# Kernel optimization log

Hardware: AMD Instinct MI355X
Metric: run time of the kernel (lower is better)

The kernel has to match this reference:

```python
import jax, jax.numpy as jnp
import numpy as np


def gru_layer(x, W_ih, W_hh, b_ih, b_hh):
    """PyTorch-semantics GRU over a full sequence.
    x: [B, T, F]; W_ih: [3H, F]; W_hh: [3H, H]; biases: [3H].
    Gate order (r, z, n) per torch.nn.GRU. Returns [B, T, H].
    """
    B, T, _ = x.shape
    H = W_hh.shape[1]
    # Precompute input projections for all timesteps as one big GEMM: [B, T, 3H]
    xg = jnp.einsum('btf,gf->btg', x, W_ih) + b_ih

    def step(h, xg_t):
        gh = h @ W_hh.T + b_hh                      # [B, 3H]
        xr, xz, xn = jnp.split(xg_t, 3, axis=-1)
        hr, hz, hn = jnp.split(gh, 3, axis=-1)
        r = jax.nn.sigmoid(xr + hr)
        z = jax.nn.sigmoid(xz + hz)
        n = jnp.tanh(xn + r * hn)
        h_new = (1.0 - z) * n + z * h
        return h_new, h_new

    h0 = jnp.zeros((B, H), dtype=x.dtype)
    _, hs = jax.lax.scan(step, h0, jnp.swapaxes(xg, 0, 1))  # hs: [T, B, H]
    return jnp.swapaxes(hs, 0, 1)


def setup_inputs() -> dict:
    key = jax.random.key(0)
    ks = jax.random.split(key, 16)
    B, T, F = 512, 256, 64
    H1, H2, H3 = 256, 128, 64

    def w(k, shape, fan_in):
        s = 1.0 / np.sqrt(fan_in)
        return jax.random.uniform(k, shape, jnp.float32, -s, s)

    return {
        'x': jax.random.normal(ks[0], (B, T, F), jnp.float32),
        'W_ih1': w(ks[1], (3 * H1, F), H1),
        'W_hh1': w(ks[2], (3 * H1, H1), H1),
        'b_ih1': w(ks[3], (3 * H1,), H1),
        'b_hh1': w(ks[4], (3 * H1,), H1),
        'W_ih2': w(ks[5], (3 * H2, H1), H2),
        'W_hh2': w(ks[6], (3 * H2, H2), H2),
        'b_ih2': w(ks[7], (3 * H2,), H2),
        'b_hh2': w(ks[8], (3 * H2,), H2),
        'W_ih3': w(ks[9], (3 * H3, H2), H3),
        'W_hh3': w(ks[10], (3 * H3, H3), H3),
        'b_ih3': w(ks[11], (3 * H3,), H3),
        'b_hh3': w(ks[12], (3 * H3,), H3),
        'W_dense': w(ks[13], (1, H3), H3),
        'b_dense': w(ks[14], (1,), H3),
    }


def reference(x, W_ih1, W_hh1, b_ih1, b_hh1,
              W_ih2, W_hh2, b_ih2, b_hh2,
              W_ih3, W_hh3, b_ih3, b_hh3,
              W_dense, b_dense):
    # Dropout layers act as identity in eval mode.
    h = gru_layer(x, W_ih1, W_hh1, b_ih1, b_hh1)   # [B, T, 256]
    h = gru_layer(h, W_ih2, W_hh2, b_ih2, b_hh2)   # [B, T, 128]
    h = gru_layer(h, W_ih3, W_hh3, b_ih3, b_hh3)   # [B, T, 64]
    last = h[:, -1, :]                              # [B, 64]
    return last @ W_dense.T + b_dense               # [B, 1]
```

## Files before the change

kernel.cpp:

```cpp
#include <hip/hip_runtime.h>
#include <cstddef>

typedef _Float16 f16x8 __attribute__((ext_vector_type(8)));
typedef _Float16 f16x4 __attribute__((ext_vector_type(4)));
typedef short    s16x8 __attribute__((ext_vector_type(8)));
typedef short    s16x4 __attribute__((ext_vector_type(4)));
typedef float    f32x4 __attribute__((ext_vector_type(4)));

#define MFMA_F16(a, b, c) __builtin_amdgcn_mfma_f32_16x16x32_f16((a), (b), (c), 0, 0, 0)

#if __has_builtin(__builtin_amdgcn_rcpf)
__device__ __forceinline__ float fast_rcp(float x) { return __builtin_amdgcn_rcpf(x); }
#else
__device__ __forceinline__ float fast_rcp(float x) { return 1.f / x; }
#endif

__device__ __forceinline__ f16x8 ld8(const short* p) {
  return __builtin_bit_cast(f16x8, *(const s16x8*)p);
}
__device__ __forceinline__ f16x4 ld4(const short* p) {
  return __builtin_bit_cast(f16x4, *(const s16x4*)p);
}

__device__ __forceinline__ void barrier_nodrain() {
  asm volatile("s_waitcnt lgkmcnt(0)" ::: "memory");
  __builtin_amdgcn_s_barrier();
  asm volatile("" ::: "memory");
}

struct CastDesc { const float* src; short* dst; int n; };
struct CastArgs { CastDesc d[7]; };

__global__ void cast_many(CastArgs a) {
  const int tid = blockIdx.x * blockDim.x + threadIdx.x;
  const int stride = gridDim.x * blockDim.x;
#pragma unroll
  for (int j = 0; j < 7; j++) {
    const float* __restrict__ s = a.d[j].src;
    short* __restrict__ o = a.d[j].dst;
    const int n = a.d[j].n;
    for (int i = tid; i < n; i += stride)
      o[i] = __builtin_bit_cast(short, (_Float16)s[i]);
  }
}

template <int K, int NO, int NW, int JT>
__global__ __launch_bounds__(NW * 64, 2)
void xg_gemm(const short* __restrict__ A,
             const short* __restrict__ W,
             const float* __restrict__ bias,
             short* __restrict__ xg,
             int t0, int TC) {
  static_assert(NW * 16 * JT == NO, "wave tiling must cover NO");
  constexpr int T = 256;
  constexpr int TT = 16;
  constexpr int KC = K / 32;
  const int lane = threadIdx.x & 63;
  const int wid  = threadIdx.x >> 6;
  const int p = lane & 15, q = lane >> 4;
  const int bt = blockIdx.x;
  const int tbeg = t0 + blockIdx.y * TT;
  const int j0 = wid * 16 * JT;

  f16x8 wb[JT][KC];
  float bc[JT];
#pragma unroll
  for (int jt = 0; jt < JT; jt++) {
    const int col = j0 + jt * 16 + p;
    bc[jt] = bias[col];
#pragma unroll
    for (int kc = 0; kc < KC; kc++)
      wb[jt][kc] = ld8(W + (size_t)col * K + kc * 32 + q * 8);
  }

  const short* arow = A + ((size_t)(bt * 16 + p) * T + tbeg) * K + q * 8;
  short* outb = xg + ((size_t)bt * TC + (tbeg - t0)) * NO * 16;

  f16x8 a0[KC], a1[KC];
#pragma unroll
  for (int kc = 0; kc < KC; kc++) a0[kc] = ld8(arow + kc * 32);

  auto step = [&](int ti, f16x8 (&ac)[KC], f16x8 (&anx)[KC], bool pf) {
    if (pf) {
#pragma unroll
      for (int kc = 0; kc < KC; kc++)
        anx[kc] = ld8(arow + (size_t)(ti + 1) * K + kc * 32);
    }
    f32x4 acc[JT];
#pragma unroll
    for (int jt = 0; jt < JT; jt++)
      acc[jt] = f32x4{bc[jt], bc[jt], bc[jt], bc[jt]};
#pragma unroll
    for (int kc = 0; kc < KC; kc++)
#pragma unroll
      for (int jt = 0; jt < JT; jt++)
        acc[jt] = MFMA_F16(ac[kc], wb[jt][kc], acc[jt]);
    short* ob = outb + (size_t)ti * NO * 16;
#pragma unroll
    for (int jt = 0; jt < JT; jt++) {
      const int col = j0 + jt * 16 + p;
      s16x4 v;
#pragma unroll
      for (int r = 0; r < 4; r++)
        v[r] = __builtin_bit_cast(short, (_Float16)acc[jt][r]);
      *(s16x4*)&ob[col * 16 + q * 4] = v;
    }
  };

#pragma unroll 1
  for (int ti = 0; ti < TT; ti += 2) {
    step(ti, a0, a1, true);
    step(ti + 1, a1, a0, ti + 2 < TT);
  }
}

template <int H, int NW, int JT, bool NLDS, bool SEQ, int XD>
__global__ __launch_bounds__(NW * 64, (NW / 4 >= 2) ? 2 : 1)
void gru_rec(const short* __restrict__ xg,
             const short* __restrict__ Whh,
             const float* __restrict__ bhh,
             short* __restrict__ hseq,
             float* __restrict__ hstate,
             int t0, int t1, int TC) {
  static_assert(NW * 16 * JT == H, "wave tiling must cover H");
  static_assert(XD == 2 || XD == 4, "XD even for static parity");
  constexpr int T = 256;
  constexpr int KS = H / 32;
  constexpr int HP = H + 8;
  constexpr int NO = 3 * H;

  extern __shared__ __align__(16) short smem[];
  short* wn = smem;
  short* hb = smem + (NLDS ? H * HP : 0);

  const int tid  = threadIdx.x;
  const int lane = tid & 63;
  const int wid  = tid >> 6;
  const int p = lane & 15, q = lane >> 4;
  const int b0 = blockIdx.x * 16;
  const int j0 = wid * 16 * JT;

  if constexpr (NLDS) {
    constexpr int KV = H / 8;
    for (int i = tid; i < H * KV; i += NW * 64) {
      const int row = i / KV, kc = i - row * KV;
      *(s16x8*)&wn[row * HP + kc * 8] =
          *(const s16x8*)&Whh[(size_t)(2 * H + row) * H + kc * 8];
    }
  }
  if (t0 == 0) {
    for (int i = tid; i < 16 * HP; i += NW * 64) hb[i] = 0;
  } else {
    for (int i = tid; i < 16 * H; i += NW * 64) {
      const int row = i / H, col = i - row * H;
      hb[row * HP + col] =
          __builtin_bit_cast(short, (_Float16)hstate[(size_t)(b0 + row) * H + col]);
    }
  }

  f16x8 wr[JT][NLDS ? 2 : 3][KS];
#pragma unroll
  for (int jt = 0; jt < JT; jt++) {
    const int col = j0 + jt * 16 + p;
#pragma unroll
    for (int g = 0; g < (NLDS ? 2 : 3); g++)
#pragma unroll
      for (int k = 0; k < KS; k++)
        wr[jt][g][k] = ld8(Whh + (size_t)(g * H + col) * H + k * 32 + q * 8);
  }
  float bhr[JT], bhz[JT], bhn[JT];
  int wrow[JT];
#pragma unroll
  for (int jt = 0; jt < JT; jt++) {
    const int col = j0 + jt * 16 + p;
    wrow[jt] = col;
    bhr[jt] = bhh[col];
    bhz[jt] = bhh[H + col];
    bhn[jt] = bhh[2 * H + col];
  }

  float hprev[JT][4];
#pragma unroll
  for (int jt = 0; jt < JT; jt++)
#pragma unroll
    for (int r = 0; r < 4; r++)
      hprev[jt][r] = (t0 == 0) ? 0.f
                   : hstate[(size_t)(b0 + q * 4 + r) * H + (j0 + jt * 16 + p)];

  const size_t sbase = (size_t)blockIdx.x * TC * NO * 16;
  int loff[JT][3];
#pragma unroll
  for (int jt = 0; jt < JT; jt++)
#pragma unroll
    for (int g = 0; g < 3; g++)
      loff[jt][g] = (g * H + j0 + jt * 16 + p) * 16 + q * 4;

  f16x4 xb[XD][JT][3];
#pragma unroll
  for (int u = 0; u < XD; u++)
#pragma unroll
    for (int jt = 0; jt < JT; jt++)
#pragma unroll
      for (int g = 0; g < 3; g++)
        xb[u][jt][g] = ld4(xg + sbase + (size_t)u * NO * 16 + loff[jt][g]);

  __syncthreads();

  const int steps = t1 - t0;
#pragma unroll 1
  for (int sb = 0; sb < steps; sb += XD) {
#pragma unroll
    for (int u = 0; u < XD; u++) {
      const int s = sb + u;
      const int t = t0 + s;
      short* hbc = hb + (u & 1) * 16 * HP;
      short* hbn = hb + ((u & 1) ^ 1) * 16 * HP;

      f32x4 ar[JT], az[JT], an[JT];
#pragma unroll
      for (int jt = 0; jt < JT; jt++) {
#pragma unroll
        for (int r = 0; r < 4; r++) {
          ar[jt][r] = (float)xb[u][jt][0][r];
          az[jt][r] = (float)xb[u][jt][1][r];
        }
        an[jt] = f32x4{0.f, 0.f, 0.f, 0.f};
      }
#pragma unroll
      for (int k = 0; k < KS; k++) {
        const f16x8 ahk = ld8(&hbc[p * HP + k * 32 + q * 8]);
#pragma unroll
        for (int jt = 0; jt < JT; jt++) {
          ar[jt] = MFMA_F16(ahk, wr[jt][0][k], ar[jt]);
          az[jt] = MFMA_F16(ahk, wr[jt][1][k], az[jt]);
          if constexpr (NLDS) {
            const f16x8 wnk = ld8(&wn[wrow[jt] * HP + k * 32 + q * 8]);
            an[jt] = MFMA_F16(ahk, wnk, an[jt]);
          } else {
            an[jt] = MFMA_F16(ahk, wr[jt][2][k], an[jt]);
          }
        }
      }
#pragma unroll
      for (int jt = 0; jt < JT; jt++) {
        const int col = j0 + jt * 16 + p;
#pragma unroll
        for (int r = 0; r < 4; r++) {
          const int bm = q * 4 + r;
          const float rpre = ar[jt][r] + bhr[jt];
          const float zpre = az[jt][r] + bhz[jt];
          const float rg = fast_rcp(1.f + __expf(-rpre));
          const float zg = fast_rcp(1.f + __expf(-zpre));
          const float xnv = (float)xb[u][jt][2][r];
          const float narg = xnv + rg * (an[jt][r] + bhn[jt]);
          const float e2 = __expf(2.f * narg);
          const float ng = 1.f - 2.f * fast_rcp(e2 + 1.f);
          const float hnew = (1.f - zg) * ng + zg * hprev[jt][r];
          hprev[jt][r] = hnew;
          const _Float16 hf = (_Float16)hnew;
          hbn[bm * HP + col] = __builtin_bit_cast(short, hf);
          if constexpr (SEQ)
            hseq[((size_t)(b0 + bm) * T + t) * H + col] = __builtin_bit_cast(short, hf);
        }
      }
      if (t == t1 - 1) {
#pragma unroll
        for (int jt = 0; jt < JT; jt++)
#pragma unroll
          for (int r = 0; r < 4; r++)
            hstate[(size_t)(b0 + q * 4 + r) * H + (j0 + jt * 16 + p)] = hprev[jt][r];
      }
      {
        const size_t s2 = sbase + (size_t)(s + XD) * NO * 16;
#pragma unroll
        for (int jt = 0; jt < JT; jt++)
#pragma unroll
          for (int g = 0; g < 3; g++)
            xb[u][jt][g] = ld4(xg + s2 + loff[jt][g]);
      }
      barrier_nodrain();
    }
  }
}

__global__ __launch_bounds__(512, 1)
void rec23(const short* __restrict__ xg2,
           const short* __restrict__ Whh2,
           const float* __restrict__ bhh2,
           const short* __restrict__ Wih3,
           const short* __restrict__ Whh3,
           const float* __restrict__ bih3,
           const float* __restrict__ bhh3,
           float* __restrict__ hs2,
           float* __restrict__ hs3,
           int t0, int t1, int TC) {
  constexpr int H2 = 128, H3 = 64;
  constexpr int HP2 = H2 + 8, HP3 = H3 + 8;
  constexpr int NO = 3 * H2;
  __shared__ __align__(16) short hb2[2][16][HP2];
  __shared__ __align__(16) short hb3[2][16][HP3];

  const int tid = threadIdx.x;
  const int lane = tid & 63, wid = tid >> 6;
  const int p = lane & 15, q = lane >> 4;
  const int bt = blockIdx.x, b0 = bt * 16;
  const int col2 = wid * 16 + p;
  const int col3 = (wid & 3) * 16 + p;
  const bool act3 = wid < 4;

  if (t0 == 0) {
    for (int i = tid; i < 2 * 16 * HP2; i += 512) (&hb2[0][0][0])[i] = 0;
    for (int i = tid; i < 2 * 16 * HP3; i += 512) (&hb3[0][0][0])[i] = 0;
  } else {
    for (int i = tid; i < 16 * H2; i += 512) {
      const int r = i / H2, c = i - r * H2;
      hb2[0][r][c] = __builtin_bit_cast(short, (_Float16)hs2[(size_t)(b0 + r) * H2 + c]);
    }
    for (int i = tid; i < 16 * H3; i += 512) {
      const int r = i / H3, c = i - r * H3;
      hb3[0][r][c] = __builtin_bit_cast(short, (_Float16)hs3[(size_t)(b0 + r) * H3 + c]);
    }
  }

  f16x8 w2[3][4];
#pragma unroll
  for (int g = 0; g < 3; g++)
#pragma unroll
    for (int k = 0; k < 4; k++)
      w2[g][k] = ld8(Whh2 + (size_t)(g * H2 + col2) * H2 + k * 32 + q * 8);
  const float br2 = bhh2[col2], bz2 = bhh2[H2 + col2], bn2 = bhh2[2 * H2 + col2];

  f16x8 wi3[3][4], wh3[3][2];
  float br3 = 0.f, bz3 = 0.f, bn3x = 0.f, bn3h = 0.f;
  if (act3) {
#pragma unroll
    for (int g = 0; g < 3; g++) {
#pragma unroll
      for (int k = 0; k < 4; k++)
        wi3[g][k] = ld8(Wih3 + (size_t)(g * H3 + col3) * H2 + k * 32 + q * 8);
#pragma unroll
      for (int k = 0; k < 2; k++)
        wh3[g][k] = ld8(Whh3 + (size_t)(g * H3 + col3) * H3 + k * 32 + q * 8);
    }
    br3 = bih3[col3] + bhh3[col3];
    bz3 = bih3[H3 + col3] + bhh3[H3 + col3];
    bn3x = bih3[2 * H3 + col3];
    bn3h = bhh3[2 * H3 + col3];
  }

  float h2p[4], h3p[4];
#pragma unroll
  for (int r = 0; r < 4; r++) {
    h2p[r] = (t0 == 0) ? 0.f : hs2[(size_t)(b0 + q * 4 + r) * H2 + col2];
    h3p[r] = (!act3 || t0 == 0) ? 0.f : hs3[(size_t)(b0 + q * 4 + r) * H3 + col3];
  }

  const size_t sbase = (size_t)bt * TC * NO * 16;
  int loff[3];
#pragma unroll
  for (int g = 0; g < 3; g++) loff[g] = (g * H2 + col2) * 16 + q * 4;
  f16x4 xb[2][3];
#pragma unroll
  for (int u = 0; u < 2; u++)
#pragma unroll
    for (int g = 0; g < 3; g++)
      xb[u][g] = ld4(xg2 + sbase + (size_t)u * NO * 16 + loff[g]);

  __syncthreads();

  const int steps = t1 - t0;
#pragma unroll 1
  for (int sb = 0; sb < steps; sb += 2) {
#pragma unroll
    for (int u = 0; u < 2; ++u) {
      const int s = sb + u;
      const int t = t0 + s;
      f32x4 ar, az, an;
#pragma unroll
      for (int r = 0; r < 4; r++) { ar[r] = (float)xb[u][0][r]; az[r] = (float)xb[u][1][r]; }
      an = f32x4{0.f, 0.f, 0.f, 0.f};
#pragma unroll
      for (int k = 0; k < 4; k++) {
        const f16x8 ahk = ld8(&hb2[u][p][k * 32 + q * 8]);
        ar = MFMA_F16(ahk, w2[0][k], ar);
        az = MFMA_F16(ahk, w2[1][k], az);
        an = MFMA_F16(ahk, w2[2][k], an);
      }
#pragma unroll
      for (int r = 0; r < 4; r++) {
        const int bm = q * 4 + r;
        const float rg = fast_rcp(1.f + __expf(-(ar[r] + br2)));
        const float zg = fast_rcp(1.f + __expf(-(az[r] + bz2)));
        const float narg = (float)xb[u][2][r] + rg * (an[r] + bn2);
        const float e2 = __expf(2.f * narg);
        const float ng = 1.f - 2.f * fast_rcp(e2 + 1.f);
        const float hnew = (1.f - zg) * ng + zg * h2p[r];
        h2p[r] = hnew;
        hb2[u ^ 1][bm][col2] = __builtin_bit_cast(short, (_Float16)hnew);
        if (t == t1 - 1) hs2[(size_t)(b0 + bm) * H2 + col2] = hnew;
      }
      {
        const size_t s2 = sbase + (size_t)(s + 2) * NO * 16;
#pragma unroll
        for (int g = 0; g < 3; g++) xb[u][g] = ld4(xg2 + s2 + loff[g]);
      }
      barrier_nodrain();
      if (act3) {
        f32x4 a3r{0.f,0.f,0.f,0.f}, a3z{0.f,0.f,0.f,0.f},
              a3x{0.f,0.f,0.f,0.f}, a3h{0.f,0.f,0.f,0.f};
#pragma unroll
        for (int k = 0; k < 4; k++) {
          const f16x8 a2k = ld8(&hb2[u ^ 1][p][k * 32 + q * 8]);
          a3r = MFMA_F16(a2k, wi3[0][k], a3r);
          a3z = MFMA_F16(a2k, wi3[1][k], a3z);
          a3x = MFMA_F16(a2k, wi3[2][k], a3x);
        }
#pragma unroll
        for (int k = 0; k < 2; k++) {
          const f16x8 a3k = ld8(&hb3[u][p][k * 32 + q * 8]);
          a3r = MFMA_F16(a3k, wh3[0][k], a3r);
          a3z = MFMA_F16(a3k, wh3[1][k], a3z);
          a3h = MFMA_F16(a3k, wh3[2][k], a3h);
        }
#pragma unroll
        for (int r = 0; r < 4; r++) {
          const int bm = q * 4 + r;
          const float rg = fast_rcp(1.f + __expf(-(a3r[r] + br3)));
          const float zg = fast_rcp(1.f + __expf(-(a3z[r] + bz3)));
          const float narg = a3x[r] + bn3x + rg * (a3h[r] + bn3h);
          const float e2 = __expf(2.f * narg);
          const float ng = 1.f - 2.f * fast_rcp(e2 + 1.f);
          const float hnew = (1.f - zg) * ng + zg * h3p[r];
          h3p[r] = hnew;
          hb3[u ^ 1][bm][col3] = __builtin_bit_cast(short, (_Float16)hnew);
          if (t == t1 - 1) hs3[(size_t)(b0 + bm) * H3 + col3] = hnew;
        }
      }
    }
  }
}

__global__ void dense_kernel(const float* __restrict__ hl, const float* __restrict__ Wd,
                             const float* __restrict__ bd, float* __restrict__ out) {
  const int b = blockIdx.x * 64 + threadIdx.x;
  float a = bd[0];
#pragma unroll
  for (int k = 0; k < 64; k++) a = fmaf(hl[b * 64 + k], Wd[k], a);
  out[b] = a;
}

extern "C" void kernel_launch(void* const* d_in, const int* in_sizes, int n_in,
                              void* d_out, int out_size, void* d_ws, size_t ws_size,
                              hipStream_t stream) {
  constexpr int B = 512, T = 256, F = 64;
  constexpr int H1 = 256, H2 = 128, H3 = 64;
  constexpr int M = B * T;

  const float* x     = (const float*)d_in[0];
  const float* W_ih1 = (const float*)d_in[1];
  const float* W_hh1 = (const float*)d_in[2];
  const float* b_ih1 = (const float*)d_in[3];
  const float* b_hh1 = (const float*)d_in[4];
  const float* W_ih2 = (const float*)d_in[5];
  const float* W_hh2 = (const float*)d_in[6];
  const float* b_ih2 = (const float*)d_in[7];
  const float* b_hh2 = (const float*)d_in[8];
  const float* W_ih3 = (const float*)d_in[9];
  const float* W_hh3 = (const float*)d_in[10];
  const float* b_ih3 = (const float*)d_in[11];
  const float* b_hh3 = (const float*)d_in[12];
  const float* W_d   = (const float*)d_in[13];
  const float* b_d   = (const float*)d_in[14];
  float* out = (float*)d_out;

  char* ws = (char*)d_ws;
  size_t off = 0;
  auto alloc = [&](size_t bytes) -> char* {
    char* pp = ws + off;
    off = (off + bytes + 255) & ~(size_t)255;
    return pp;
  };

  const int nx    = M * F;
  const int nwih1 = 3 * H1 * F,  nwhh1 = 3 * H1 * H1;
  const int nwih2 = 3 * H2 * H1, nwhh2 = 3 * H2 * H2;
  const int nwih3 = 3 * H3 * H2, nwhh3 = 3 * H3 * H3;

  short* xh   = (short*)alloc((size_t)nx * 2);
  short* wih1 = (short*)alloc((size_t)nwih1 * 2);
  short* whh1 = (short*)alloc((size_t)nwhh1 * 2);
  short* wih2 = (short*)alloc((size_t)nwih2 * 2);
  short* whh2 = (short*)alloc((size_t)nwhh2 * 2);
  short* wih3 = (short*)alloc((size_t)nwih3 * 2);
  short* whh3 = (short*)alloc((size_t)nwhh3 * 2);
  short* h1   = (short*)alloc((size_t)M * H1 * 2);
  float* hs1  = (float*)alloc((size_t)B * H1 * 4);
  float* hs2  = (float*)alloc((size_t)B * H2 * 4);
  float* hs3  = (float*)alloc((size_t)B * H3 * 4);
  short* xgbuf = (short*)(ws + off);
  const size_t avail = (ws_size > off) ? (ws_size - off) : 0;
  (void)n_in; (void)in_sizes; (void)out_size;

  CastArgs ca;
  ca.d[0] = {x, xh, nx};
  ca.d[1] = {W_ih1, wih1, nwih1};
  ca.d[2] = {W_hh1, whh1, nwhh1};
  ca.d[3] = {W_ih2, wih2, nwih2};
  ca.d[4] = {W_hh2, whh2, nwhh2};
  ca.d[5] = {W_ih3, wih3, nwih3};
  ca.d[6] = {W_hh3, whh3, nwhh3};
  cast_many<<<1024, 256, 0, stream>>>(ca);

  auto pick_tc = [&](int NO, int XD) -> int {
    for (int tc = T; tc >= 32; tc >>= 1) {
      size_t need = (size_t)(B / 16) * tc * NO * 16 * 2
                  + (size_t)XD * NO * 16 * 2 + 256;
      if (need <= avail) return tc;
    }
    return 16;
  };

  constexpr int SM1 = (H1 + 2 * 16) * (H1 + 8) * 2;
  auto* r1 = gru_rec<H1, 8, 2, true, true, 2>;
  (void)hipFuncSetAttribute((const void*)r1, hipFuncAttributeMaxDynamicSharedMemorySize, SM1);

  {
    const int TC = pick_tc(3 * H1, 2);
    for (int t0 = 0; t0 < T; t0 += TC) {
      xg_gemm<F, 3 * H1, 4, 12><<<dim3(B / 16, TC / 16), 4 * 64, 0, stream>>>(
          xh, wih1, b_ih1, xgbuf, t0, TC);
      r1<<<B / 16, 8 * 64, SM1, stream>>>(xgbuf, whh1, b_hh1, h1, hs1, t0, t0 + TC, TC);
    }
  }
  {
    const int TC = pick_tc(3 * H2, 2);
    for (int t0 = 0; t0 < T; t0 += TC) {
      xg_gemm<H1, 3 * H2, 8, 3><<<dim3(B / 16, TC / 16), 8 * 64, 0, stream>>>(
          h1, wih2, b_ih2, xgbuf, t0, TC);
      rec23<<<B / 16, 512, 0, stream>>>(xgbuf, whh2, b_hh2, wih3, whh3, b_ih3, b_hh3,
                                        hs2, hs3, t0, t0 + TC, TC);
    }
  }

  dense_kernel<<<B / 64, 64, 0, stream>>>(hs3, W_d, b_d, out);
}
```

Baseline: 946.9 us.

## Overlap next-chunk input GEMM with recurrence via fused kernels and double-buffered ring

Fuses the input-projection GEMM for chunk c+1 into the same launch as the recurrence for chunk c. Extra blocks compute the next xg slot into a two-slot ring buffer while 32 blocks run the serial GRU recurrence, so the GEMM work fills otherwise idle CUs. It also folds b_ih and b_hh for the r/z gates into a combined bias computed in the cast kernel, removing per-step bias adds. In layer 1 it keeps the first four K-chunks of the n-gate weights in registers and the rest in LDS, which shrinks shared memory per block. The cost is higher register and LDS pressure in the fused kernel and a fixed chunk size of 64 steps.

```diff
diff --git a/kernel.cpp b/kernel.cpp
--- a/kernel.cpp
+++ b/kernel.cpp
@@ -9,6 +9,9 @@
 
 #define MFMA_F16(a, b, c) __builtin_amdgcn_mfma_f32_16x16x32_f16((a), (b), (c), 0, 0, 0)
 
+constexpr int GB = 512, GT = 256, GF = 64;
+constexpr int H1 = 256, H2 = 128, H3 = 64;
+
 #if __has_builtin(__builtin_amdgcn_rcpf)
 __device__ __forceinline__ float fast_rcp(float x) { return __builtin_amdgcn_rcpf(x); }
 #else
@@ -29,7 +32,11 @@
 }
 
 struct CastDesc { const float* src; short* dst; int n; };
-struct CastArgs { CastDesc d[7]; };
+struct CastArgs {
+  CastDesc d[7];
+  const float* bih1; const float* bhh1; float* bc1;
+  const float* bih2; const float* bhh2; float* bc2;
+};
 
 __global__ void cast_many(CastArgs a) {
   const int tid = blockIdx.x * blockDim.x + threadIdx.x;
@@ -42,24 +49,22 @@
     for (int i = tid; i < n; i += stride)
       o[i] = __builtin_bit_cast(short, (_Float16)s[i]);
   }
-}
-
-template <int K, int NO, int NW, int JT>
-__global__ __launch_bounds__(NW * 64, 2)
-void xg_gemm(const short* __restrict__ A,
-             const short* __restrict__ W,
-             const float* __restrict__ bias,
-             short* __restrict__ xg,
-             int t0, int TC) {
-  static_assert(NW * 16 * JT == NO, "wave tiling must cover NO");
-  constexpr int T = 256;
+  for (int i = tid; i < 3 * H1; i += stride)
+    a.bc1[i] = a.bih1[i] + (i < 2 * H1 ? a.bhh1[i] : 0.f);
+  for (int i = tid; i < 3 * H2; i += stride)
+    a.bc2[i] = a.bih2[i] + (i < 2 * H2 ? a.bhh2[i] : 0.f);
+}
+
+template <int K, int NO, int JT>
+__device__ __forceinline__ void g_body(const short* __restrict__ A,
+                                       const short* __restrict__ W,
+                                       const float* __restrict__ biasC,
+                                       short* __restrict__ slot, int TC,
+                                       int bt, int trel, int tabs, int tid) {
+  constexpr int KC = K / 32;
   constexpr int TT = 16;
-  constexpr int KC = K / 32;
-  const int lane = threadIdx.x & 63;
-  const int wid  = threadIdx.x >> 6;
+  const int lane = tid & 63, wid = tid >> 6;
   const int p = lane & 15, q = lane >> 4;
-  const int bt = blockIdx.x;
-  const int tbeg = t0 + blockIdx.y * TT;
   const int j0 = wid * 16 * JT;
 
   f16x8 wb[JT][KC];
@@ -67,14 +72,13 @@
 #pragma unroll
   for (int jt = 0; jt < JT; jt++) {
     const int col = j0 + jt * 16 + p;
-    bc[jt] = bias[col];
+    bc[jt] = biasC[col];
 #pragma unroll
     for (int kc = 0; kc < KC; kc++)
       wb[jt][kc] = ld8(W + (size_t)col * K + kc * 32 + q * 8);
   }
-
-  const short* arow = A + ((size_t)(bt * 16 + p) * T + tbeg) * K + q * 8;
-  short* outb = xg + ((size_t)bt * TC + (tbeg - t0)) * NO * 16;
+  const short* arow = A + ((size_t)(bt * 16 + p) * GT + tabs) * K + q * 8;
+  short* outb = slot + ((size_t)bt * TC + trel) * NO * 16;
 
   f16x8 a0[KC], a1[KC];
 #pragma unroll
@@ -114,68 +118,67 @@
   }
 }
 
-template <int H, int NW, int JT, bool NLDS, bool SEQ, int XD>
-__global__ __launch_bounds__(NW * 64, (NW / 4 >= 2) ? 2 : 1)
-void gru_rec(const short* __restrict__ xg,
-             const short* __restrict__ Whh,
-             const float* __restrict__ bhh,
-             short* __restrict__ hseq,
-             float* __restrict__ hstate,
-             int t0, int t1, int TC) {
-  static_assert(NW * 16 * JT == H, "wave tiling must cover H");
-  static_assert(XD == 2 || XD == 4, "XD even for static parity");
-  constexpr int T = 256;
-  constexpr int KS = H / 32;
-  constexpr int HP = H + 8;
-  constexpr int NO = 3 * H;
-
-  extern __shared__ __align__(16) short smem[];
+template <int K, int NO, int JT>
+__global__ __launch_bounds__(512, 2)
+void g_kern(const short* __restrict__ A, const short* __restrict__ W,
+            const float* __restrict__ biasC, short* __restrict__ slot,
+            int TC, int tbase) {
+  const int nty = TC / 16;
+  const int bt = blockIdx.x / nty, ty = blockIdx.x - bt * nty;
+  g_body<K, NO, JT>(A, W, biasC, slot, TC, bt, ty * 16, tbase + ty * 16, threadIdx.x);
+}
+
+__device__ __forceinline__ void r1_run(const short* __restrict__ xg,
+                                       const short* __restrict__ Whh,
+                                       const float* __restrict__ bhh,
+                                       short* __restrict__ hseq,
+                                       float* __restrict__ hstate,
+                                       int bt, int t0, int t1, int TC,
+                                       short* smem, int tid) {
+  constexpr int H = H1, KS = H / 32, KREG = 4, JT = 2;
+  constexpr int HP = H + 8, NO = 3 * H;
+  constexpr int KLDS = KS - KREG, WNP = KLDS * 32 + 8;
+
   short* wn = smem;
-  short* hb = smem + (NLDS ? H * HP : 0);
-
-  const int tid  = threadIdx.x;
-  const int lane = tid & 63;
-  const int wid  = tid >> 6;
+  short* hb = smem + H * WNP;
+
+  const int lane = tid & 63, wid = tid >> 6;
   const int p = lane & 15, q = lane >> 4;
-  const int b0 = blockIdx.x * 16;
-  const int j0 = wid * 16 * JT;
-
-  if constexpr (NLDS) {
-    constexpr int KV = H / 8;
-    for (int i = tid; i < H * KV; i += NW * 64) {
+  const int b0 = bt * 16, j0 = wid * 16 * JT;
+
+  {
+    constexpr int KV = KLDS * 4;
+    for (int i = tid; i < H * KV; i += 512) {
       const int row = i / KV, kc = i - row * KV;
-      *(s16x8*)&wn[row * HP + kc * 8] =
-          *(const s16x8*)&Whh[(size_t)(2 * H + row) * H + kc * 8];
+      *(s16x8*)&wn[row * WNP + kc * 8] =
+          *(const s16x8*)&Whh[(size_t)(2 * H + row) * H + KREG * 32 + kc * 8];
     }
   }
   if (t0 == 0) {
-    for (int i = tid; i < 16 * HP; i += NW * 64) hb[i] = 0;
+    for (int i = tid; i < 2 * 16 * HP; i += 512) hb[i] = 0;
   } else {
-    for (int i = tid; i < 16 * H; i += NW * 64) {
+    for (int i = tid; i < 16 * H; i += 512) {
       const int row = i / H, col = i - row * H;
       hb[row * HP + col] =
           __builtin_bit_cast(short, (_Float16)hstate[(size_t)(b0 + row) * H + col]);
     }
   }
 
-  f16x8 wr[JT][NLDS ? 2 : 3][KS];
+  f16x8 wrz[JT][2][KS], wnr[JT][KREG];
+  float bhn[JT];
+  int wrow[JT];
 #pragma unroll
   for (int jt = 0; jt < JT; jt++) {
     const int col = j0 + jt * 16 + p;
 #pragma unroll
-    for (int g = 0; g < (NLDS ? 2 : 3); g++)
+    for (int g = 0; g < 2; g++)
 #pragma unroll
       for (int k = 0; k < KS; k++)
-        wr[jt][g][k] = ld8(Whh + (size_t)(g * H + col) * H + k * 32 + q * 8);
-  }
-  float bhr[JT], bhz[JT], bhn[JT];
-  int wrow[JT];
-#pragma unroll
-  for (int jt = 0; jt < JT; jt++) {
-    const int col = j0 + jt * 16 + p;
+        wrz[jt][g][k] = ld8(Whh + (size_t)(g * H + col) * H + k * 32 + q * 8);
+#pragma unroll
+    for (int k = 0; k < KREG; k++)
+      wnr[jt][k] = ld8(Whh + (size_t)(2 * H + col) * H + k * 32 + q * 8);
     wrow[jt] = col;
-    bhr[jt] = bhh[col];
-    bhz[jt] = bhh[H + col];
     bhn[jt] = bhh[2 * H + col];
   }
 
@@ -187,7 +190,7 @@
       hprev[jt][r] = (t0 == 0) ? 0.f
                    : hstate[(size_t)(b0 + q * 4 + r) * H + (j0 + jt * 16 + p)];
 
-  const size_t sbase = (size_t)blockIdx.x * TC * NO * 16;
+  const size_t sbase = (size_t)bt * TC * NO * 16;
   int loff[JT][3];
 #pragma unroll
   for (int jt = 0; jt < JT; jt++)
@@ -195,9 +198,9 @@
     for (int g = 0; g < 3; g++)
       loff[jt][g] = (g * H + j0 + jt * 16 + p) * 16 + q * 4;
 
-  f16x4 xb[XD][JT][3];
-#pragma unroll
-  for (int u = 0; u < XD; u++)
+  f16x4 xb[2][JT][3];
+#pragma unroll
+  for (int u = 0; u < 2; u++)
 #pragma unroll
     for (int jt = 0; jt < JT; jt++)
 #pragma unroll
@@ -208,13 +211,12 @@
 
   const int steps = t1 - t0;
 #pragma unroll 1
-  for (int sb = 0; sb < steps; sb += XD) {
-#pragma unroll
-    for (int u = 0; u < XD; u++) {
-      const int s = sb + u;
-      const int t = t0 + s;
-      short* hbc = hb + (u & 1) * 16 * HP;
-      short* hbn = hb + ((u & 1) ^ 1) * 16 * HP;
+  for (int sb = 0; sb < steps; sb += 2) {
+#pragma unroll
+    for (int u = 0; u < 2; u++) {
+      const int s = sb + u, t = t0 + s;
+      short* hbc = hb + u * 16 * HP;
+      short* hbn = hb + (u ^ 1) * 16 * HP;
 
       f32x4 ar[JT], az[JT], an[JT];
 #pragma unroll
@@ -231,13 +233,13 @@
         const f16x8 ahk = ld8(&hbc[p * HP + k * 32 + q * 8]);
 #pragma unroll
         for (int jt = 0; jt < JT; jt++) {
-          ar[jt] = MFMA_F16(ahk, wr[jt][0][k], ar[jt]);
-          az[jt] = MFMA_F16(ahk, wr[jt][1][k], az[jt]);
-          if constexpr (NLDS) {
-            const f16x8 wnk = ld8(&wn[wrow[jt] * HP + k * 32 + q * 8]);
+          ar[jt] = MFMA_F16(ahk, wrz[jt][0][k], ar[jt]);
+          az[jt] = MFMA_F16(ahk, wrz[jt][1][k], az[jt]);
+          if (k < KREG) {
+            an[jt] = MFMA_F16(ahk, wnr[jt][k < KREG ? k : 0], an[jt]);
+          } else {
+            const f16x8 wnk = ld8(&wn[wrow[jt] * WNP + (k - KREG) * 32 + q * 8]);
             an[jt] = MFMA_F16(ahk, wnk, an[jt]);
-          } else {
-            an[jt] = MFMA_F16(ahk, wr[jt][2][k], an[jt]);
           }
         }
       }
@@ -247,20 +249,16 @@
 #pragma unroll
         for (int r = 0; r < 4; r++) {
           const int bm = q * 4 + r;
-          const float rpre = ar[jt][r] + bhr[jt];
-          const float zpre = az[jt][r] + bhz[jt];
-          const float rg = fast_rcp(1.f + __expf(-rpre));
-          const float zg = fast_rcp(1.f + __expf(-zpre));
-          const float xnv = (float)xb[u][jt][2][r];
-          const float narg = xnv + rg * (an[jt][r] + bhn[jt]);
+          const float rg = fast_rcp(1.f + __expf(-ar[jt][r]));
+          const float zg = fast_rcp(1.f + __expf(-az[jt][r]));
+          const float narg = (float)xb[u][jt][2][r] + rg * (an[jt][r] + bhn[jt]);
           const float e2 = __expf(2.f * narg);
           const float ng = 1.f - 2.f * fast_rcp(e2 + 1.f);
           const float hnew = (1.f - zg) * ng + zg * hprev[jt][r];
           hprev[jt][r] = hnew;
           const _Float16 hf = (_Float16)hnew;
           hbn[bm * HP + col] = __builtin_bit_cast(short, hf);
-          if constexpr (SEQ)
-            hseq[((size_t)(b0 + bm) * T + t) * H + col] = __builtin_bit_cast(short, hf);
+          hseq[((size_t)(b0 + bm) * GT + t) * H + col] = __builtin_bit_cast(short, hf);
         }
       }
       if (t == t1 - 1) {
@@ -271,7 +269,7 @@
             hstate[(size_t)(b0 + q * 4 + r) * H + (j0 + jt * 16 + p)] = hprev[jt][r];
       }
       {
-        const size_t s2 = sbase + (size_t)(s + XD) * NO * 16;
+        const size_t s2 = sbase + (size_t)(s + 2) * NO * 16;
 #pragma unroll
         for (int jt = 0; jt < JT; jt++)
 #pragma unroll
@@ -283,42 +281,39 @@
   }
 }
 
-__global__ __launch_bounds__(512, 1)
-void rec23(const short* __restrict__ xg2,
-           const short* __restrict__ Whh2,
-           const float* __restrict__ bhh2,
-           const short* __restrict__ Wih3,
-           const short* __restrict__ Whh3,
-           const float* __restrict__ bih3,
-           const float* __restrict__ bhh3,
-           float* __restrict__ hs2,
-           float* __restrict__ hs3,
-           int t0, int t1, int TC) {
-  constexpr int H2 = 128, H3 = 64;
-  constexpr int HP2 = H2 + 8, HP3 = H3 + 8;
-  constexpr int NO = 3 * H2;
-  __shared__ __align__(16) short hb2[2][16][HP2];
-  __shared__ __align__(16) short hb3[2][16][HP3];
-
-  const int tid = threadIdx.x;
+__device__ __forceinline__ void rec23_run(const short* __restrict__ xg2,
+                                          const short* __restrict__ Whh2,
+                                          const float* __restrict__ bhh2,
+                                          const short* __restrict__ Wih3,
+                                          const short* __restrict__ Whh3,
+                                          const float* __restrict__ bih3,
+                                          const float* __restrict__ bhh3,
+                                          float* __restrict__ hs2,
+                                          float* __restrict__ hs3,
+                                          int bt, int t0, int t1, int TC,
+                                          short* smem, int tid) {
+  constexpr int HP2 = H2 + 8, HP3 = H3 + 8, NO = 3 * H2;
+  short* hb2 = smem;
+  short* hb3 = smem + 2 * 16 * HP2;
+
   const int lane = tid & 63, wid = tid >> 6;
   const int p = lane & 15, q = lane >> 4;
-  const int bt = blockIdx.x, b0 = bt * 16;
+  const int b0 = bt * 16;
   const int col2 = wid * 16 + p;
   const int col3 = (wid & 3) * 16 + p;
   const bool act3 = wid < 4;
 
   if (t0 == 0) {
-    for (int i = tid; i < 2 * 16 * HP2; i += 512) (&hb2[0][0][0])[i] = 0;
-    for (int i = tid; i < 2 * 16 * HP3; i += 512) (&hb3[0][0][0])[i] = 0;
+    for (int i = tid; i < 2 * 16 * HP2; i += 512) hb2[i] = 0;
+    for (int i = tid; i < 2 * 16 * HP3; i += 512) hb3[i] = 0;
   } else {
     for (int i = tid; i < 16 * H2; i += 512) {
       const int r = i / H2, c = i - r * H2;
-      hb2[0][r][c] = __builtin_bit_cast(short, (_Float16)hs2[(size_t)(b0 + r) * H2 + c]);
+      hb2[r * HP2 + c] = __builtin_bit_cast(short, (_Float16)hs2[(size_t)(b0 + r) * H2 + c]);
     }
     for (int i = tid; i < 16 * H3; i += 512) {
       const int r = i / H3, c = i - r * H3;
-      hb3[0][r][c] = __builtin_bit_cast(short, (_Float16)hs3[(size_t)(b0 + r) * H3 + c]);
+      hb3[r * HP3 + c] = __builtin_bit_cast(short, (_Float16)hs3[(size_t)(b0 + r) * H3 + c]);
     }
   }
 
@@ -328,7 +323,7 @@
 #pragma unroll
     for (int k = 0; k < 4; k++)
       w2[g][k] = ld8(Whh2 + (size_t)(g * H2 + col2) * H2 + k * 32 + q * 8);
-  const float br2 = bhh2[col2], bz2 = bhh2[H2 + col2], bn2 = bhh2[2 * H2 + col2];
+  const float bn2 = bhh2[2 * H2 + col2];
 
   f16x8 wi3[3][4], wh3[3][2];
   float br3 = 0.f, bz3 = 0.f, bn3x = 0.f, bn3h = 0.f;
@@ -373,15 +368,14 @@
   for (int sb = 0; sb < steps; sb += 2) {
 #pragma unroll
     for (int u = 0; u < 2; ++u) {
-      const int s = sb + u;
-      const int t = t0 + s;
+      const int s = sb + u, t = t0 + s;
       f32x4 ar, az, an;
 #pragma unroll
       for (int r = 0; r < 4; r++) { ar[r] = (float)xb[u][0][r]; az[r] = (float)xb[u][1][r]; }
       an = f32x4{0.f, 0.f, 0.f, 0.f};
 #pragma unroll
       for (int k = 0; k < 4; k++) {
-        const f16x8 ahk = ld8(&hb2[u][p][k * 32 + q * 8]);
+        const f16x8 ahk = ld8(&hb2[(u * 16 + p) * HP2 + k * 32 + q * 8]);
         ar = MFMA_F16(ahk, w2[0][k], ar);
         az = MFMA_F16(ahk, w2[1][k], az);
         an = MFMA_F16(ahk, w2[2][k], an);
@@ -389,14 +383,14 @@
 #pragma unroll
       for (int r = 0; r < 4; r++) {
         const int bm = q * 4 + r;
-        const float rg = fast_rcp(1.f + __expf(-(ar[r] + br2)));
-        const float zg = fast_rcp(1.f + __expf(-(az[r] + bz2)));
+        const float rg = fast_rcp(1.f + __expf(-ar[r]));
+        const float zg = fast_rcp(1.f + __expf(-az[r]));
         const float narg = (float)xb[u][2][r] + rg * (an[r] + bn2);
         const float e2 = __expf(2.f * narg);
         const float ng = 1.f - 2.f * fast_rcp(e2 + 1.f);
         const float hnew = (1.f - zg) * ng + zg * h2p[r];
         h2p[r] = hnew;
-        hb2[u ^ 1][bm][col2] = __builtin_bit_cast(short, (_Float16)hnew);
+        hb2[((u ^ 1) * 16 + bm) * HP2 + col2] = __builtin_bit_cast(short, (_Float16)hnew);
         if (t == t1 - 1) hs2[(size_t)(b0 + bm) * H2 + col2] = hnew;
       }
       {
@@ -410,14 +404,14 @@
               a3x{0.f,0.f,0.f,0.f}, a3h{0.f,0.f,0.f,0.f};
 #pragma unroll
         for (int k = 0; k < 4; k++) {
-          const f16x8 a2k = ld8(&hb2[u ^ 1][p][k * 32 + q * 8]);
+          const f16x8 a2k = ld8(&hb2[((u ^ 1) * 16 + p) * HP2 + k * 32 + q * 8]);
           a3r = MFMA_F16(a2k, wi3[0][k], a3r);
           a3z = MFMA_F16(a2k, wi3[1][k], a3z);
           a3x = MFMA_F16(a2k, wi3[2][k], a3x);
         }
 #pragma unroll
         for (int k = 0; k < 2; k++) {
-          const f16x8 a3k = ld8(&hb3[u][p][k * 32 + q * 8]);
+          const f16x8 a3k = ld8(&hb3[(u * 16 + p) * HP3 + k * 32 + q * 8]);
           a3r = MFMA_F16(a3k, wh3[0][k], a3r);
           a3z = MFMA_F16(a3k, wh3[1][k], a3z);
           a3h = MFMA_F16(a3k, wh3[2][k], a3h);
@@ -432,11 +426,48 @@
           const float ng = 1.f - 2.f * fast_rcp(e2 + 1.f);
           const float hnew = (1.f - zg) * ng + zg * h3p[r];
           h3p[r] = hnew;
-          hb3[u ^ 1][bm][col3] = __builtin_bit_cast(short, (_Float16)hnew);
+          hb3[((u ^ 1) * 16 + bm) * HP3 + col3] = __builtin_bit_cast(short, (_Float16)hnew);
           if (t == t1 - 1) hs3[(size_t)(b0 + bm) * H3 + col3] = hnew;
         }
       }
     }
+  }
+}
+
+__global__ __launch_bounds__(512, 2)
+void fused1(const short* __restrict__ xg_rd, short* __restrict__ xg_wr,
+            const short* __restrict__ xh, const short* __restrict__ wih1,
+            const float* __restrict__ bc1, const short* __restrict__ whh1,
+            const float* __restrict__ bhh1, short* __restrict__ h1,
+            float* __restrict__ hs1, int t0, int TC) {
+  extern __shared__ __align__(16) short smem[];
+  if (blockIdx.x < 32) {
+    r1_run(xg_rd, whh1, bhh1, h1, hs1, blockIdx.x, t0, t0 + TC, TC, smem, threadIdx.x);
+  } else if (xg_wr) {
+    const int g = blockIdx.x - 32, nty = TC / 16;
+    const int bt = g / nty, ty = g - bt * nty;
+    g_body<GF, 3 * H1, 6>(xh, wih1, bc1, xg_wr, TC, bt, ty * 16,
+                          t0 + TC + ty * 16, threadIdx.x);
+  }
+}
+
+__global__ __launch_bounds__(512, 2)
+void fused2(const short* __restrict__ xg_rd, short* __restrict__ xg_wr,
+            const short* __restrict__ h1, const short* __restrict__ wih2,
+            const float* __restrict__ bc2, const short* __restrict__ whh2,
+            const float* __restrict__ bhh2, const short* __restrict__ wih3,
+            const short* __restrict__ whh3, const float* __restrict__ bih3,
+            const float* __restrict__ bhh3, float* __restrict__ hs2,
+            float* __restrict__ hs3, int t0, int TC) {
+  extern __shared__ __align__(16) short smem[];
+  if (blockIdx.x < 32) {
+    rec23_run(xg_rd, whh2, bhh2, wih3, whh3, bih3, bhh3, hs2, hs3,
+              blockIdx.x, t0, t0 + TC, TC, smem, threadIdx.x);
+  } else if (xg_wr) {
+    const int g = blockIdx.x - 32, nty = TC / 16;
+    const int bt = g / nty, ty = g - bt * nty;
+    g_body<H1, 3 * H2, 3>(h1, wih2, bc2, xg_wr, TC, bt, ty * 16,
+                          t0 + TC + ty * 16, threadIdx.x);
   }
 }
 
@@ -452,8 +483,7 @@
 extern "C" void kernel_launch(void* const* d_in, const int* in_sizes, int n_in,
                               void* d_out, int out_size, void* d_ws, size_t ws_size,
                               hipStream_t stream) {
-  constexpr int B = 512, T = 256, F = 64;
-  constexpr int H1 = 256, H2 = 128, H3 = 64;
+  constexpr int B = GB, T = GT, F = GF;
   constexpr int M = B * T;
 
   const float* x     = (const float*)d_in[0];
@@ -497,9 +527,21 @@
   float* hs1  = (float*)alloc((size_t)B * H1 * 4);
   float* hs2  = (float*)alloc((size_t)B * H2 * 4);
   float* hs3  = (float*)alloc((size_t)B * H3 * 4);
-  short* xgbuf = (short*)(ws + off);
+  float* bc1  = (float*)alloc(3 * H1 * 4);
+  float* bc2  = (float*)alloc(3 * H2 * 4);
+  (void)n_in; (void)in_sizes; (void)out_size;
+
   const size_t avail = (ws_size > off) ? (ws_size - off) : 0;
-  (void)n_in; (void)in_sizes; (void)out_size;
+  int TC = 64;
+  auto need = [&](int tc) -> size_t {
+    return (size_t)tc * 1572864  + (size_t)tc * 786432  + 2 * 65536;
+  };
+  while (TC > 16 && need(TC) > avail) TC >>= 1;
+  const int NC = T / TC, nty = TC / 16;
+  const size_t slot1e = (size_t)32 * TC * (3 * H1) * 16;
+  const size_t slot2e = (size_t)32 * TC * (3 * H2) * 16;
+  short* ring1 = (short*)alloc(2 * slot1e * 2 + 65536);
+  short* ring2 = (short*)alloc(2 * slot2e * 2 + 65536);
 
   CastArgs ca;
   ca.d[0] = {x, xh, nx};
@@ -509,37 +551,29 @@
   ca.d[4] = {W_hh2, whh2, nwhh2};
   ca.d[5] = {W_ih3, wih3, nwih3};
   ca.d[6] = {W_hh3, whh3, nwhh3};
+  ca.bih1 = b_ih1; ca.bhh1 = b_hh1; ca.bc1 = bc1;
+  ca.bih2 = b_ih2; ca.bhh2 = b_hh2; ca.bc2 = bc2;
   cast_many<<<1024, 256, 0, stream>>>(ca);
 
-  auto pick_tc = [&](int NO, int XD) -> int {
-    for (int tc = T; tc >= 32; tc >>= 1) {
-      size_t need = (size_t)(B / 16) * tc * NO * 16 * 2
-                  + (size_t)XD * NO * 16 * 2 + 256;
-      if (need <= avail) return tc;
-    }
-    return 16;
-  };
-
-  constexpr int SM1 = (H1 + 2 * 16) * (H1 + 8) * 2;
-  auto* r1 = gru_rec<H1, 8, 2, true, true, 2>;
-  (void)hipFuncSetAttribute((const void*)r1, hipFuncAttributeMaxDynamicSharedMemorySize, SM1);
-
-  {
-    const int TC = pick_tc(3 * H1, 2);
-    for (int t0 = 0; t0 < T; t0 += TC) {
-      xg_gemm<F, 3 * H1, 4, 12><<<dim3(B / 16, TC / 16), 4 * 64, 0, stream>>>(
-          xh, wih1, b_ih1, xgbuf, t0, TC);
-      r1<<<B / 16, 8 * 64, SM1, stream>>>(xgbuf, whh1, b_hh1, h1, hs1, t0, t0 + TC, TC);
-    }
-  }
-  {
-    const int TC = pick_tc(3 * H2, 2);
-    for (int t0 = 0; t0 < T; t0 += TC) {
-      xg_gemm<H1, 3 * H2, 8, 3><<<dim3(B / 16, TC / 16), 8 * 64, 0, stream>>>(
-          h1, wih2, b_ih2, xgbuf, t0, TC);
-      rec23<<<B / 16, 512, 0, stream>>>(xgbuf, whh2, b_hh2, wih3, whh3, b_ih3, b_hh3,
-                                        hs2, hs3, t0, t0 + TC, TC);
-    }
+  constexpr int SM1 = H1 * 136 * 2 + 2 * 16 * (H1 + 8) * 2;
+  constexpr int SM2 = 2 * 16 * (H2 + 8) * 2 + 2 * 16 * (H3 + 8) * 2;
+  (void)hipFuncSetAttribute((const void*)fused1,
+                            hipFuncAttributeMaxDynamicSharedMemorySize, SM1);
+
+  g_kern<GF, 3 * H1, 6><<<32 * nty, 512, 0, stream>>>(xh, wih1, bc1, ring1, TC, 0);
+  for (int c = 0; c < NC; ++c) {
+    const short* rd = ring1 + (size_t)(c & 1) * slot1e;
+    short* wr = (c + 1 < NC) ? ring1 + (size_t)((c + 1) & 1) * slot1e : nullptr;
+    fused1<<<32 + (wr ? 32 * nty : 0), 512, SM1, stream>>>(
+        rd, wr, xh, wih1, bc1, whh1, b_hh1, h1, hs1, c * TC, TC);
+  }
+  g_kern<H1, 3 * H2, 3><<<32 * nty, 512, 0, stream>>>(h1, wih2, bc2, ring2, TC, 0);
+  for (int c = 0; c < NC; ++c) {
+    const short* rd = ring2 + (size_t)(c & 1) * slot2e;
+    short* wr = (c + 1 < NC) ? ring2 + (size_t)((c + 1) & 1) * slot2e : nullptr;
+    fused2<<<32 + (wr ? 32 * nty : 0), 512, SM2, stream>>>(
+        rd, wr, h1, wih2, bc2, whh2, b_hh2, wih3, whh3, b_ih3, b_hh3,
+        hs2, hs3, c * TC, TC);
   }
 
   dense_kernel<<<B / 64, 64, 0, stream>>>(hs3, W_d, b_d, out);
```

After: 1.278 ms. 1.35x slower.
